# Kernel tuning notes

Measured on AMD Instinct MI355X. Metric: run time of the kernel, lower is better.

Reference implementation:

```python
import jax, jax.numpy as jnp
import numpy as np

# dims (match init_kwargs)
L, D, H, K = 8, 384, 6, 64            # layers, hidden, rwkv heads, rwkv head dim
DI, MH, HD, DS, CK = 768, 12, 64, 64, 4  # mamba: d_inner, heads, head_dim, d_state, conv kernel
V, B, T = 32000, 1, 1024


def _rms(x, w, eps=1e-6):
    return w * x * jax.lax.rsqrt(jnp.mean(x * x, axis=-1, keepdims=True) + eps)


def _rwkv6(xn, Wr, Wk, Wv, Wg, Ww, w_bias, u, gn_w, gn_b, Wo):
    # RWKV6: data-dependent diagonal-decay linear attention
    Bb, Tt, Dd = xn.shape
    proj = lambda W: (xn @ W).reshape(Bb, Tt, H, K)
    r, k, v = proj(Wr), proj(Wk), proj(Wv)
    g = xn @ Wg                                        # [B,T,D]
    w = (xn @ Ww + w_bias).reshape(Bb, Tt, H, K)
    decay = jnp.exp(-jnp.exp(w))                       # in (0,1)

    def step(S, inp):                                  # S: [B,H,K,K] (key x value)
        r_t, k_t, v_t, d_t = inp                       # each [B,H,K]
        kv = k_t[..., :, None] * v_t[..., None, :]     # [B,H,K,K]
        o = jnp.einsum('bhk,bhkv->bhv', r_t, S + u[None, :, :, None] * kv)
        S = d_t[..., None] * S + kv
        return S, o

    tm = lambda a: jnp.moveaxis(a, 1, 0)               # time-major
    S0 = jnp.zeros((Bb, H, K, K), xn.dtype)
    _, o = jax.lax.scan(step, S0, (tm(r), tm(k), tm(v), tm(decay)))
    o = jnp.moveaxis(o, 0, 1)                          # [B,T,H,K]
    # per-head GroupNorm
    mu = jnp.mean(o, -1, keepdims=True)
    var = jnp.var(o, -1, keepdims=True)
    o = (o - mu) * jax.lax.rsqrt(var + 1e-5) * gn_w.reshape(H, K) + gn_b.reshape(H, K)
    o = o.reshape(Bb, Tt, Dd) * jax.nn.silu(g)
    return o @ Wo


def _mamba2(xn, W_in, conv_w, conv_b, dt_bias, A_log, Dp, mn_w, W_out):
    # Mamba2: selective scan with scalar A per head
    Bb, Tt, Dd = xn.shape
    zxbcdt = xn @ W_in                                 # [B,T, 2*DI + 2*DS + MH]
    z = zxbcdt[..., :DI]
    xBC = zxbcdt[..., DI:DI + DI + 2 * DS]
    dt = jax.nn.softplus(zxbcdt[..., -MH:] + dt_bias)  # [B,T,MH]
    # causal depthwise conv1d, kernel CK
    xp = jnp.pad(xBC, ((0, 0), (CK - 1, 0), (0, 0)))
    xBC = sum(xp[:, j:j + Tt, :] * conv_w[:, j] for j in range(CK)) + conv_b
    xBC = jax.nn.silu(xBC)
    xs = xBC[..., :DI].reshape(Bb, Tt, MH, HD)
    Bm = xBC[..., DI:DI + DS]                          # [B,T,DS]
    Cm = xBC[..., DI + DS:]                            # [B,T,DS]
    A = -jnp.exp(A_log)                                # [MH]

    def step(S, inp):                                  # S: [B,MH,HD,DS]
        x_t, B_t, C_t, dt_t = inp                      # [B,MH,HD],[B,DS],[B,DS],[B,MH]
        dA = jnp.exp(dt_t * A)                         # [B,MH]
        S = dA[..., None, None] * S + (dt_t[..., None] * x_t)[..., None] * B_t[:, None, None, :]
        y = jnp.einsum('bhps,bs->bhp', S, C_t) + Dp[None, :, None] * x_t
        return S, y

    tm = lambda a: jnp.moveaxis(a, 1, 0)
    S0 = jnp.zeros((Bb, MH, HD, DS), xn.dtype)
    _, y = jax.lax.scan(step, S0, (tm(xs), tm(Bm), tm(Cm), tm(dt)))
    y = jnp.moveaxis(y, 0, 1).reshape(Bb, Tt, DI)
    y = _rms(y * jax.nn.silu(z), mn_w)                 # gated RMSNorm
    return y @ W_out


def _forward(x, embed, ln_w, Wr, Wk, Wv, Wg, Ww, w_bias, u, gn_w, gn_b, Wo,
             W_in, conv_w, conv_b, dt_bias, A_log, Dp, mn_w, W_out,
             gw, gb, ffn_ln_w, ffn_w1, ffn_w2, ln_out_w):
    h = jnp.take(embed, x, axis=0)                     # [B,T,D]
    for i in range(L):
        xn = _rms(h, ln_w[i])
        o_r = _rwkv6(xn, Wr[i], Wk[i], Wv[i], Wg[i], Ww[i], w_bias[i], u[i], gn_w[i], gn_b[i], Wo[i])
        o_m = _mamba2(xn, W_in[i], conv_w[i], conv_b[i], dt_bias[i], A_log[i], Dp[i], mn_w[i], W_out[i])
        gate = jax.nn.sigmoid(jnp.concatenate([o_r, o_m], -1) @ gw[i] + gb[i])  # [B,T,1]
        h = h + gate * o_r + (1.0 - gate) * o_m
        hn = _rms(h, ffn_ln_w[i])
        h = h + jax.nn.gelu(hn @ ffn_w1[i], approximate=False) @ ffn_w2[i]
    h = _rms(h, ln_out_w)
    return h @ embed.T                                 # tied head -> [B,T,V]


def setup_inputs() -> dict:
    key = jax.random.key(0)
    ks = iter(jax.random.split(key, 32))
    n = lambda shape, s=0.02: jax.random.normal(next(ks), shape, jnp.float32) * s
    d = {}
    d['x'] = jax.random.randint(next(ks), (B, T), 0, V)
    d['embed'] = n((V, D))
    d['ln_w'] = jnp.ones((L, D), jnp.float32)
    d['Wr'] = n((L, D, D)); d['Wk'] = n((L, D, D)); d['Wv'] = n((L, D, D))
    d['Wg'] = n((L, D, D)); d['Ww'] = n((L, D, D))
    d['w_bias'] = n((L, D), 0.5)
    d['u'] = n((L, H, K), 0.5)
    d['gn_w'] = jnp.ones((L, D), jnp.float32)
    d['gn_b'] = jnp.zeros((L, D), jnp.float32)
    d['Wo'] = n((L, D, D))
    d['W_in'] = n((L, D, 2 * DI + 2 * DS + MH))
    d['conv_w'] = n((L, DI + 2 * DS, CK), 0.2)
    d['conv_b'] = jnp.zeros((L, DI + 2 * DS), jnp.float32)
    d['dt_bias'] = jax.random.uniform(next(ks), (L, MH), jnp.float32, -4.0, -1.0)
    d['A_log'] = jnp.log(jax.random.uniform(next(ks), (L, MH), jnp.float32, 1.0, 16.0))
    d['Dp'] = jnp.ones((L, MH), jnp.float32)
    d['mn_w'] = jnp.ones((L, DI), jnp.float32)
    d['W_out'] = n((L, DI, D))
    d['gw'] = n((L, 2 * D, 1), 0.01)
    d['gb'] = jnp.full((L, 1), float(np.log(0.3 / 0.7)), jnp.float32)
    d['ffn_ln_w'] = jnp.ones((L, D), jnp.float32)
    d['ffn_w1'] = n((L, D, 4 * D))
    d['ffn_w2'] = n((L, 4 * D, D))
    d['ln_out_w'] = jnp.ones((D,), jnp.float32)
    return d


def reference(x, embed, ln_w, Wr, Wk, Wv, Wg, Ww, w_bias, u, gn_w, gn_b, Wo,
              W_in, conv_w, conv_b, dt_bias, A_log, Dp, mn_w, W_out,
              gw, gb, ffn_ln_w, ffn_w1, ffn_w2, ln_out_w):
    return _forward(x, embed, ln_w, Wr, Wk, Wv, Wg, Ww, w_bias, u, gn_w, gn_b, Wo,
                    W_in, conv_w, conv_b, dt_bias, A_log, Dp, mn_w, W_out,
                    gw, gb, ffn_ln_w, ffn_w1, ffn_w2, ln_out_w)
```

## Files before the change

### kernel.cpp

```cpp
#include <hip/hip_runtime.h>
#include <math.h>

#define TT 1024
#define DD 384
#define NH 6
#define DI 768
#define MH 12
#define DS 64
#define NL 8
#define XDIM 1676
#define CONVC 896
#define NV 32000
#define PZS 3712
#define G_OFF 1152
#define W_OFF 1536
#define Z_OFF 1920
#define XBC_OFF 2688
#define DT_OFF 3584
#define CHK 32
#define NCH 32

typedef __attribute__((ext_vector_type(8))) short short8;
typedef __attribute__((ext_vector_type(4))) float f32x4;

__device__ __forceinline__ float siluf(float x) { return x / (1.f + expf(-x)); }
__device__ __forceinline__ float sigmoidf_(float x) { return 1.f / (1.f + expf(-x)); }
__device__ __forceinline__ float geluf(float x) {
  return 0.5f * x * (1.f + erff(x * 0.70710678118654752440f));
}
__device__ __forceinline__ unsigned short f2b(float x) {
  union { float f; unsigned int u; } v; v.f = x;
  unsigned int r = v.u + 0x7fffu + ((v.u >> 16) & 1u);
  return (unsigned short)(r >> 16);
}

#define GLDS(gp, lp) __builtin_amdgcn_global_load_lds( \
    (const __attribute__((address_space(1))) void*)(gp), \
    (__attribute__((address_space(3))) void*)(lp), 16, 0, 0)

template<int EPI>
__global__ __launch_bounds__(256) void gemm_bf16(
    const unsigned short* __restrict__ A, const unsigned short* __restrict__ Bt,
    float* __restrict__ C, unsigned short* __restrict__ Cb, int N, int K, int ldC)
{
  __shared__ unsigned short As[2048];
  __shared__ unsigned short Bs[2048];
  int tid = threadIdx.x;
  int wid = tid >> 6, lane = tid & 63;
  int m0 = blockIdx.y * 64, n0 = blockIdx.x * 64;
  int wr = wid >> 1, wc = wid & 1;
  int sr = tid >> 2;
  int scs = ((tid & 3) ^ ((sr >> 1) & 3)) * 8;
  const unsigned short* ga = A  + (size_t)(m0 + sr) * K + scs;
  const unsigned short* gb = Bt + (size_t)(n0 + sr) * K + scs;
  unsigned short* la = As + wid * 512;
  unsigned short* lb = Bs + wid * 512;
  int fr = lane & 15, fc = lane >> 4;
  f32x4 zz = {0.f, 0.f, 0.f, 0.f};
  f32x4 acc[2][2];
  acc[0][0] = zz; acc[0][1] = zz; acc[1][0] = zz; acc[1][1] = zz;

  for (int k0 = 0; k0 < K; k0 += 32) {
    GLDS(ga + k0, la);
    GLDS(gb + k0, lb);
    __syncthreads();
    short8 af[2], bf[2];
#pragma unroll
    for (int mg = 0; mg < 2; ++mg) {
      int ar = wr * 32 + mg * 16 + fr;
      af[mg] = *reinterpret_cast<const short8*>(&As[ar * 32 + ((fc ^ ((ar >> 1) & 3)) * 8)]);
    }
#pragma unroll
    for (int ng = 0; ng < 2; ++ng) {
      int br = wc * 32 + ng * 16 + fr;
      bf[ng] = *reinterpret_cast<const short8*>(&Bs[br * 32 + ((fc ^ ((br >> 1) & 3)) * 8)]);
    }
#pragma unroll
    for (int mg = 0; mg < 2; ++mg)
#pragma unroll
      for (int ng = 0; ng < 2; ++ng)
        acc[mg][ng] = __builtin_amdgcn_mfma_f32_16x16x32_bf16(af[mg], bf[ng], acc[mg][ng], 0, 0, 0);
    __syncthreads();
  }
#pragma unroll
  for (int mg = 0; mg < 2; ++mg)
#pragma unroll
    for (int ng = 0; ng < 2; ++ng) {
      int col = n0 + wc * 32 + ng * 16 + fr;
      if (col < N) {
#pragma unroll
        for (int j = 0; j < 4; ++j) {
          int row = m0 + wr * 32 + mg * 16 + fc * 4 + j;
          if (EPI == 1)      Cb[(size_t)row * ldC + col] = f2b(geluf(acc[mg][ng][j]));
          else if (EPI == 2) C[(size_t)row * ldC + col] += acc[mg][ng][j];
          else               C[(size_t)row * ldC + col]  = acc[mg][ng][j];
        }
      }
    }
}

__global__ __launch_bounds__(256) void gemm128(
    const unsigned short* __restrict__ A, const unsigned short* __restrict__ Bt,
    float* __restrict__ C, int N, int K, int ldC)
{
  __shared__ unsigned short As[4096];
  __shared__ unsigned short Bs[4096];
  int tid = threadIdx.x;
  int wid = tid >> 6, lane = tid & 63;
  int m0 = blockIdx.y * 128, n0 = blockIdx.x * 128;
  int wr = wid >> 1, wc = wid & 1;
  int r0 = tid >> 2;
  int scs = ((tid & 3) ^ ((r0 >> 1) & 3)) * 8;
  const unsigned short* ga0 = A  + (size_t)(m0 + r0) * K + scs;
  const unsigned short* gb0 = Bt + (size_t)(n0 + r0) * K + scs;
  const unsigned short* ga1 = ga0 + (size_t)64 * K;
  const unsigned short* gb1 = gb0 + (size_t)64 * K;
  unsigned short* la0 = As + wid * 512;
  unsigned short* lb0 = Bs + wid * 512;
  unsigned short* la1 = As + 2048 + wid * 512;
  unsigned short* lb1 = Bs + 2048 + wid * 512;
  int fr = lane & 15, fc = lane >> 4;
  f32x4 zz = {0.f, 0.f, 0.f, 0.f};
  f32x4 acc[4][4];
#pragma unroll
  for (int i = 0; i < 4; i++)
#pragma unroll
    for (int j = 0; j < 4; j++) acc[i][j] = zz;

  for (int k0 = 0; k0 < K; k0 += 32) {
    GLDS(ga0 + k0, la0);
    GLDS(gb0 + k0, lb0);
    GLDS(ga1 + k0, la1);
    GLDS(gb1 + k0, lb1);
    __syncthreads();
    short8 af[4], bf[4];
#pragma unroll
    for (int mg = 0; mg < 4; ++mg) {
      int ar = wr * 64 + mg * 16 + fr;
      af[mg] = *reinterpret_cast<const short8*>(&As[ar * 32 + ((fc ^ ((ar >> 1) & 3)) * 8)]);
    }
#pragma unroll
    for (int ng = 0; ng < 4; ++ng) {
      int br = wc * 64 + ng * 16 + fr;
      bf[ng] = *reinterpret_cast<const short8*>(&Bs[br * 32 + ((fc ^ ((br >> 1) & 3)) * 8)]);
    }
#pragma unroll
    for (int mg = 0; mg < 4; ++mg)
#pragma unroll
      for (int ng = 0; ng < 4; ++ng)
        acc[mg][ng] = __builtin_amdgcn_mfma_f32_16x16x32_bf16(af[mg], bf[ng], acc[mg][ng], 0, 0, 0);
    __syncthreads();
  }
#pragma unroll
  for (int mg = 0; mg < 4; ++mg)
#pragma unroll
    for (int ng = 0; ng < 4; ++ng) {
      int col = n0 + wc * 64 + ng * 16 + fr;
      if (col < N) {
#pragma unroll
        for (int j = 0; j < 4; ++j) {
          int row = m0 + wr * 64 + mg * 16 + fc * 4 + j;
          C[(size_t)row * ldC + col] = acc[mg][ng][j];
        }
      }
    }
}

__global__ __launch_bounds__(256) void transconv_kernel(
    const float* __restrict__ src, unsigned short* __restrict__ dst,
    int K, int N, int Npad, size_t srcStride, size_t dstStride)
{
  __shared__ float tile[32][33];
  src += (size_t)blockIdx.z * srcStride;
  dst += (size_t)blockIdx.z * dstStride;
  int k0 = blockIdx.y * 32, n0 = blockIdx.x * 32;
  int tx = threadIdx.x & 31, ty = threadIdx.x >> 5;
  for (int i = ty; i < 32; i += 8) {
    int k = k0 + i, n = n0 + tx;
    tile[i][tx] = (k < K && n < N) ? src[(size_t)k * N + n] : 0.f;
  }
  __syncthreads();
  for (int i = ty; i < 32; i += 8) {
    int n = n0 + i, k = k0 + tx;
    if (n < Npad && k < K) dst[(size_t)n * K + k] = f2b(tile[tx][i]);
  }
}

__global__ void conv_b16_kernel(const float* __restrict__ src, unsigned short* __restrict__ dst, int n)
{
  int idx = blockIdx.x * 256 + threadIdx.x;
  if (idx < n) dst[idx] = f2b(src[idx]);
}

__global__ void embed_kernel(const int* __restrict__ x, const float* __restrict__ embed,
                             float* __restrict__ h)
{
  int idx = blockIdx.x * 256 + threadIdx.x;
  if (idx < TT * DD) {
    int t = idx / DD, d = idx % DD;
    h[idx] = embed[(size_t)x[t] * DD + d];
  }
}

__global__ __launch_bounds__(256) void rms_kernel(const float* __restrict__ in,
                                                  const float* __restrict__ w,
                                                  unsigned short* __restrict__ out,
                                                  int ncol, float eps)
{
  int t = blockIdx.x;
  const float* row = in + (size_t)t * ncol;
  float ss = 0.f;
  for (int c = threadIdx.x; c < ncol; c += 256) { float v = row[c]; ss = fmaf(v, v, ss); }
  __shared__ float red[256];
  red[threadIdx.x] = ss; __syncthreads();
  for (int s = 128; s > 0; s >>= 1) {
    if (threadIdx.x < s) red[threadIdx.x] += red[threadIdx.x + s];
    __syncthreads();
  }
  float scale = rsqrtf(red[0] / ncol + eps);
  for (int c = threadIdx.x; c < ncol; c += 256) out[(size_t)t * ncol + c] = f2b(w[c] * row[c] * scale);
}

__global__ __launch_bounds__(256) void scanA_kernel(
    const float* __restrict__ PZ, const float* __restrict__ u, const float* __restrict__ wbias,
    float* __restrict__ so, float* __restrict__ rPb,
    float* __restrict__ MstR, float* __restrict__ DcR,
    const float* __restrict__ xbc, const float* __restrict__ dtbias,
    const float* __restrict__ Alog, const float* __restrict__ Dpw,
    float* __restrict__ yb, float* __restrict__ Ccb,
    float* __restrict__ MstM, float* __restrict__ DcM)
{
  __shared__ float smem[2 * 256 + 64];
  int b = blockIdx.x, tid = threadIdx.x;
  if (b < 192) {
    int h = b >> 5, c = b & 31;
    float* sbuf = smem; float* us = smem + 512;
    if (tid < 64) us[tid] = u[h * 64 + tid];
    int wv = tid >> 6, l = tid & 63;
    int vv = wv * 16 + (l & 15);
    int kc = l >> 4;
    int arr = tid >> 6, idx = tid & 63;
    int off = (arr == 0) ? 0 : (arr == 1) ? 384 : (arr == 2) ? W_OFF : 768;
    float wb = (arr == 2) ? wbias[h * 64 + idx] : 0.f;
    size_t base = (size_t)h * 64 + idx + off;
    int t0 = c * CHK;
    float S[16], Pc[16];
#pragma unroll
    for (int i = 0; i < 16; i++) { S[i] = 0.f; Pc[i] = 1.f; }
    float reg = PZ[(size_t)t0 * PZS + base];
    bool st = (wv == 0) && ((l & 15) == 0);
    for (int t = 0; t < CHK; ++t) {
      int tt = t0 + t;
      float* cb = sbuf + (t & 1) * 256;
      cb[arr * 64 + idx] = (arr == 2) ? expf(-expf(reg + wb)) : reg;
      if (t + 1 < CHK) reg = PZ[(size_t)(tt + 1) * PZS + base];
      __syncthreads();
      float vt = cb[192 + vv];
      float acc = 0.f;
      float rp[16];
#pragma unroll
      for (int i = 0; i < 16; ++i) {
        int kk = kc * 16 + i;
        float rv = cb[kk], kv = cb[64 + kk], dv = cb[128 + kk];
        rp[i] = rv * Pc[i];
        float kvv = kv * vt;
        acc = fmaf(rv, fmaf(us[kk], kvv, S[i]), acc);
        S[i] = fmaf(dv, S[i], kvv);
        Pc[i] *= dv;
      }
      acc += __shfl_xor(acc, 16);
      acc += __shfl_xor(acc, 32);
      if (l < 16) so[(size_t)tt * DD + h * 64 + vv] = acc;
      if (st) {
        float4* dst = (float4*)&rPb[(size_t)tt * DD + h * 64 + kc * 16];
        dst[0] = make_float4(rp[0], rp[1], rp[2], rp[3]);
        dst[1] = make_float4(rp[4], rp[5], rp[6], rp[7]);
        dst[2] = make_float4(rp[8], rp[9], rp[10], rp[11]);
        dst[3] = make_float4(rp[12], rp[13], rp[14], rp[15]);
      }
    }
    float* ms = MstR + (size_t)(h * NCH + c) * 4096;
    float4* msv = (float4*)&ms[vv * 64 + kc * 16];
    msv[0] = make_float4(S[0], S[1], S[2], S[3]);
    msv[1] = make_float4(S[4], S[5], S[6], S[7]);
    msv[2] = make_float4(S[8], S[9], S[10], S[11]);
    msv[3] = make_float4(S[12], S[13], S[14], S[15]);
    if (st) {
      float4* dd_ = (float4*)&DcR[(h * NCH + c) * 64 + kc * 16];
      dd_[0] = make_float4(Pc[0], Pc[1], Pc[2], Pc[3]);
      dd_[1] = make_float4(Pc[4], Pc[5], Pc[6], Pc[7]);
      dd_[2] = make_float4(Pc[8], Pc[9], Pc[10], Pc[11]);
      dd_[3] = make_float4(Pc[12], Pc[13], Pc[14], Pc[15]);
    }
  } else {
    int bb = b - 192;
    int hh = bb >> 5, c = bb & 31;
    float* sbuf = smem;
    int wv = tid >> 6, l = tid & 63;
    int p = wv * 16 + (l & 15);
    int sc = l >> 4;
    int arr = tid >> 6, idx = tid & 63;
    float A = -expf(Alog[hh]);
    float Dph = Dpw[hh];
    float dtbh = dtbias[hh];
    int off = (arr == 0) ? (hh * 64 + idx) : (arr == 1) ? (DI + idx) : (DI + DS + idx);
    int t0 = c * CHK;
    float S[16]; float cdA = 1.f;
#pragma unroll
    for (int i = 0; i < 16; i++) S[i] = 0.f;
    float reg = (arr < 3) ? xbc[(size_t)t0 * CONVC + off]
                          : PZ[(size_t)t0 * PZS + DT_OFF + hh];
    bool st = (wv == 0) && ((l & 15) == 0);
    for (int t = 0; t < CHK; ++t) {
      int tt = t0 + t;
      float* cb = sbuf + (t & 1) * 256;
      if (arr < 3) cb[arr * 64 + idx] = reg;
      else if (idx == 0) {
        float v = reg + dtbh;
        cb[192] = (v > 20.f) ? v : log1pf(expf(v));
      }
      if (t + 1 < CHK) reg = (arr < 3) ? xbc[(size_t)(tt + 1) * CONVC + off]
                                       : PZ[(size_t)(tt + 1) * PZS + DT_OFF + hh];
      __syncthreads();
      float dt_ = cb[192];
      float dA = expf(dt_ * A);
      cdA *= dA;
      float xp = cb[p];
      float dtx = dt_ * xp;
      float acc = 0.f;
#pragma unroll
      for (int i = 0; i < 16; ++i) {
        int s = sc * 16 + i;
        S[i] = fmaf(dA, S[i], dtx * cb[64 + s]);
        acc = fmaf(S[i], cb[128 + s], acc);
      }
      acc += __shfl_xor(acc, 16);
      acc += __shfl_xor(acc, 32);
      if (l < 16) yb[(size_t)tt * DI + hh * 64 + p] = fmaf(Dph, xp, acc);
      if (st) {
        float4* dst = (float4*)&Ccb[(size_t)tt * DI + hh * 64 + sc * 16];
#pragma unroll
        for (int j4 = 0; j4 < 4; ++j4)
          dst[j4] = make_float4(cdA * cb[128 + sc * 16 + j4 * 4 + 0],
                                cdA * cb[128 + sc * 16 + j4 * 4 + 1],
                                cdA * cb[128 + sc * 16 + j4 * 4 + 2],
                                cdA * cb[128 + sc * 16 + j4 * 4 + 3]);
      }
    }
    float* ms = MstM + (size_t)(hh * NCH + c) * 4096;
    float4* msv = (float4*)&ms[p * 64 + sc * 16];
    msv[0] = make_float4(S[0], S[1], S[2], S[3]);
    msv[1] = make_float4(S[4], S[5], S[6], S[7]);
    msv[2] = make_float4(S[8], S[9], S[10], S[11]);
    msv[3] = make_float4(S[12], S[13], S[14], S[15]);
    if (tid == 0) DcM[hh * NCH + c] = cdA;
  }
}

__global__ __launch_bounds__(256) void combine_kernel(
    const float* __restrict__ MstR, const float* __restrict__ DcR, float* __restrict__ S0R,
    const float* __restrict__ MstM, const float* __restrict__ DcM, float* __restrict__ S0M)
{
  int b = blockIdx.x, tid = threadIdx.x;
  if (b < 96) {
    int h = b >> 4, sub = b & 15;
    int ei = sub * 256 + tid;
    int k = ei & 63;
    float S = 0.f;
#pragma unroll
    for (int c = 0; c < NCH; ++c) {
      size_t base = (size_t)(h * NCH + c) * 4096;
      float m = MstR[base + ei];
      float dD = DcR[(h * NCH + c) * 64 + k];
      S0R[base + ei] = S;
      S = fmaf(dD, S, m);
    }
  } else {
    int bb = b - 96;
    int hh = bb >> 4, sub = bb & 15;
    int ei = sub * 256 + tid;
    float S = 0.f;
#pragma unroll
    for (int c = 0; c < NCH; ++c) {
      size_t base = (size_t)(hh * NCH + c) * 4096;
      float m = MstM[base + ei];
      float dD = DcM[hh * NCH + c];
      S0M[base + ei] = S;
      S = fmaf(dD, S, m);
    }
  }
}

__global__ __launch_bounds__(256) void corr_kernel(
    const float* __restrict__ S0R, const float* __restrict__ rPb, const float* __restrict__ so,
    const float* __restrict__ S0M, const float* __restrict__ Ccb, float* __restrict__ yb,
    const float* __restrict__ PZ, const float* __restrict__ gnw, const float* __restrict__ gnb,
    unsigned short* __restrict__ gob)
{
  __shared__ float S0l[64 * 68];
  __shared__ float Rl[CHK * 68];
  int b = blockIdx.x, tid = threadIdx.x;
  const float* s0g; const float* rg; int ostride, obase, t0;
  bool rwkv = (b < 192);
  int h;
  if (rwkv) {
    h = b >> 5; int c = b & 31; t0 = c * CHK;
    s0g = S0R + (size_t)(h * NCH + c) * 4096;
    rg = rPb; obase = h * 64; ostride = DD;
  } else {
    int bb = b - 192; h = bb >> 5; int c = bb & 31; t0 = c * CHK;
    s0g = S0M + (size_t)(h * NCH + c) * 4096;
    rg = Ccb; obase = h * 64; ostride = DI;
  }
  for (int gi = tid; gi < 4096; gi += 256)
    S0l[(gi & 63) * 68 + (gi >> 6)] = s0g[gi];
  {
    int t = tid >> 3, q = (tid & 7) * 8;
    const float4* src = (const float4*)&rg[(size_t)(t0 + t) * ostride + obase + q];
    float4* dst = (float4*)&Rl[t * 68 + q];
    dst[0] = src[0]; dst[1] = src[1];
  }
  __syncthreads();
  int t = tid >> 3, q = (tid & 7) * 8;
  float acc[8];
#pragma unroll
  for (int j = 0; j < 8; j++) acc[j] = 0.f;
  for (int k = 0; k < 64; ++k) {
    float rv = Rl[t * 68 + k];
    const float4* sp = (const float4*)&S0l[k * 68 + q];
    float4 s0 = sp[0], s1 = sp[1];
    acc[0] = fmaf(rv, s0.x, acc[0]);
    acc[1] = fmaf(rv, s0.y, acc[1]);
    acc[2] = fmaf(rv, s0.z, acc[2]);
    acc[3] = fmaf(rv, s0.w, acc[3]);
    acc[4] = fmaf(rv, s1.x, acc[4]);
    acc[5] = fmaf(rv, s1.y, acc[5]);
    acc[6] = fmaf(rv, s1.z, acc[6]);
    acc[7] = fmaf(rv, s1.w, acc[7]);
  }
  if (!rwkv) {
    float4* op = (float4*)&yb[(size_t)(t0 + t) * DI + obase + q];
    float4 c0 = op[0], c1 = op[1];
    c0.x += acc[0]; c0.y += acc[1]; c0.z += acc[2]; c0.w += acc[3];
    c1.x += acc[4]; c1.y += acc[5]; c1.z += acc[6]; c1.w += acc[7];
    op[0] = c0; op[1] = c1;
  } else {
    float ov[8];
    const float4* sp = (const float4*)&so[(size_t)(t0 + t) * DD + obase + q];
    float4 s0 = sp[0], s1 = sp[1];
    ov[0] = s0.x + acc[0]; ov[1] = s0.y + acc[1]; ov[2] = s0.z + acc[2]; ov[3] = s0.w + acc[3];
    ov[4] = s1.x + acc[4]; ov[5] = s1.y + acc[5]; ov[6] = s1.z + acc[6]; ov[7] = s1.w + acc[7];
    float m_ = 0.f;
#pragma unroll
    for (int j = 0; j < 8; j++) m_ += ov[j];
    m_ += __shfl_xor(m_, 1); m_ += __shfl_xor(m_, 2); m_ += __shfl_xor(m_, 4);
    float mu = m_ * (1.f / 64.f);
    float vv = 0.f;
#pragma unroll
    for (int j = 0; j < 8; j++) { float d = ov[j] - mu; vv = fmaf(d, d, vv); }
    vv += __shfl_xor(vv, 1); vv += __shfl_xor(vv, 2); vv += __shfl_xor(vv, 4);
    float rstd = rsqrtf(vv * (1.f / 64.f) + 1e-5f);
#pragma unroll
    for (int j = 0; j < 8; j++) {
      int d = obase + q + j;
      float gv = PZ[(size_t)(t0 + t) * PZS + G_OFF + d];
      float o = fmaf((ov[j] - mu) * rstd, gnw[d], gnb[d]) * siluf(gv);
      gob[(size_t)(t0 + t) * DD + d] = f2b(o);
    }
  }
}

__global__ void conv_kernel(const float* __restrict__ PZ, const float* __restrict__ cw,
                            const float* __restrict__ cb, float* __restrict__ out)
{
  int idx = blockIdx.x * 256 + threadIdx.x;
  if (idx >= TT * CONVC) return;
  int t = idx / CONVC, c = idx % CONVC;
  float acc = cb[c];
#pragma unroll
  for (int j = 0; j < 4; ++j) {
    int tt = t + j - 3;
    if (tt >= 0) acc = fmaf(PZ[(size_t)tt * PZS + XBC_OFF + c], cw[c * 4 + j], acc);
  }
  out[idx] = siluf(acc);
}

__global__ __launch_bounds__(256) void mamba_norm_kernel(const float* __restrict__ yb,
    const float* __restrict__ PZ, const float* __restrict__ mnw, unsigned short* __restrict__ out)
{
  int t = blockIdx.x;
  __shared__ float vbuf[DI];
  __shared__ float red[256];
  float ss = 0.f;
  for (int c = threadIdx.x; c < DI; c += 256) {
    float z = PZ[(size_t)t * PZS + Z_OFF + c];
    float v = yb[(size_t)t * DI + c] * siluf(z);
    vbuf[c] = v;
    ss = fmaf(v, v, ss);
  }
  red[threadIdx.x] = ss; __syncthreads();
  for (int s = 128; s > 0; s >>= 1) {
    if (threadIdx.x < s) red[threadIdx.x] += red[threadIdx.x + s];
    __syncthreads();
  }
  float scale = rsqrtf(red[0] / DI + 1e-6f);
  for (int c = threadIdx.x; c < DI; c += 256)
    out[(size_t)t * DI + c] = f2b(vbuf[c] * scale * mnw[c]);
}

__global__ __launch_bounds__(256) void gate_rms_kernel(const float* __restrict__ orb,
    const float* __restrict__ omb, const float* __restrict__ gw,
    const float* __restrict__ gb, const float* __restrict__ flnw,
    float* __restrict__ h, unsigned short* __restrict__ xnb)
{
  int t = blockIdx.x;
  __shared__ float red[256];
  __shared__ float vbuf[DD];
  float ss = 0.f;
  for (int c = threadIdx.x; c < DD; c += 256)
    ss += orb[(size_t)t * DD + c] * gw[c] + omb[(size_t)t * DD + c] * gw[DD + c];
  red[threadIdx.x] = ss; __syncthreads();
  for (int s = 128; s > 0; s >>= 1) {
    if (threadIdx.x < s) red[threadIdx.x] += red[threadIdx.x + s];
    __syncthreads();
  }
  float gate = sigmoidf_(red[0] + gb[0]);
  __syncthreads();
  float ss2 = 0.f;
  for (int c = threadIdx.x; c < DD; c += 256) {
    size_t ix = (size_t)t * DD + c;
    float hn = h[ix] + gate * orb[ix] + (1.f - gate) * omb[ix];
    h[ix] = hn; vbuf[c] = hn;
    ss2 = fmaf(hn, hn, ss2);
  }
  red[threadIdx.x] = ss2; __syncthreads();
  for (int s = 128; s > 0; s >>= 1) {
    if (threadIdx.x < s) red[threadIdx.x] += red[threadIdx.x + s];
    __syncthreads();
  }
  float scale = rsqrtf(red[0] / DD + 1e-6f);
  for (int c = threadIdx.x; c < DD; c += 256)
    xnb[(size_t)t * DD + c] = f2b(flnw[c] * vbuf[c] * scale);
}

extern "C" void kernel_launch(void* const* d_in, const int* in_sizes, int n_in,
                              void* d_out, int out_size, void* d_ws, size_t ws_size,
                              hipStream_t stream)
{
  const int*   x        = (const int*)  d_in[0];
  const float* embed    = (const float*)d_in[1];
  const float* ln_w     = (const float*)d_in[2];
  const float* Wr       = (const float*)d_in[3];
  const float* Wk       = (const float*)d_in[4];
  const float* Wv       = (const float*)d_in[5];
  const float* Wg       = (const float*)d_in[6];
  const float* Ww       = (const float*)d_in[7];
  const float* w_bias   = (const float*)d_in[8];
  const float* u        = (const float*)d_in[9];
  const float* gn_w     = (const float*)d_in[10];
  const float* gn_b     = (const float*)d_in[11];
  const float* Wo       = (const float*)d_in[12];
  const float* W_in     = (const float*)d_in[13];
  const float* conv_w   = (const float*)d_in[14];
  const float* conv_b   = (const float*)d_in[15];
  const float* dt_bias  = (const float*)d_in[16];
  const float* A_log    = (const float*)d_in[17];
  const float* Dp       = (const float*)d_in[18];
  const float* mn_w     = (const float*)d_in[19];
  const float* W_out    = (const float*)d_in[20];
  const float* gw       = (const float*)d_in[21];
  const float* gb       = (const float*)d_in[22];
  const float* ffn_ln_w = (const float*)d_in[23];
  const float* ffn_w1   = (const float*)d_in[24];
  const float* ffn_w2   = (const float*)d_in[25];
  const float* ln_out_w = (const float*)d_in[26];

  char* base = (char*)d_ws;
  size_t off = 0;
  auto alloc = [&](size_t bytes) { off = (off + 255) & ~(size_t)255; void* p = base + off; off += bytes; return p; };

  float* h    = (float*)alloc((size_t)TT * DD * 4);
  float* PZ   = (float*)alloc((size_t)TT * PZS * 4);
  float* xb   = (float*)alloc((size_t)TT * CONVC * 4);
  float* yb   = (float*)alloc((size_t)TT * DI * 4);
  float* so   = (float*)alloc((size_t)TT * DD * 4);
  float* orb  = (float*)alloc((size_t)TT * DD * 4);
  float* omb  = (float*)alloc((size_t)TT * DD * 4);
  float* rPb  = (float*)alloc((size_t)TT * DD * 4);
  float* Ccb  = (float*)alloc((size_t)TT * DI * 4);
  float* MstR = (float*)alloc((size_t)NH * NCH * 4096 * 4);
  float* DcR  = (float*)alloc((size_t)NH * NCH * 64 * 4);
  float* S0R  = (float*)alloc((size_t)NH * NCH * 4096 * 4);
  float* MstM = (float*)alloc((size_t)MH * NCH * 4096 * 4);
  float* DcM  = (float*)alloc((size_t)MH * NCH * 4);
  float* S0M  = (float*)alloc((size_t)MH * NCH * 4096 * 4);
  unsigned short* xnb = (unsigned short*)alloc((size_t)TT * DD * 2);
  unsigned short* gob = (unsigned short*)alloc((size_t)TT * DD * 2);
  unsigned short* ynb = (unsigned short*)alloc((size_t)TT * DI * 2);
  unsigned short* fhb = (unsigned short*)alloc((size_t)TT * 1536 * 2);
  unsigned short* WallT = (unsigned short*)alloc((size_t)NL * PZS * 384 * 2);
  unsigned short* WoT   = (unsigned short*)alloc((size_t)NL * 384 * 384 * 2);
  unsigned short* WoutT = (unsigned short*)alloc((size_t)NL * 384 * 768 * 2);
  unsigned short* F1T   = (unsigned short*)alloc((size_t)NL * 1536 * 384 * 2);
  unsigned short* F2T   = (unsigned short*)alloc((size_t)NL * 384 * 1536 * 2);
  unsigned short* embB  = (unsigned short*)alloc((size_t)NV * DD * 2);
  (void)ws_size; (void)in_sizes; (void)n_in; (void)out_size;

  dim3 blk(256);
  int gTD = (TT * DD + 255) / 256;

  const float* Wrkvgw[5] = {Wr, Wk, Wv, Wg, Ww};
  for (int j = 0; j < 5; ++j)
    transconv_kernel<<<dim3(12, 12, 8), blk, 0, stream>>>(
        Wrkvgw[j], WallT + (size_t)j * 384 * 384, 384, 384, 384,
        (size_t)384 * 384, (size_t)PZS * 384);
  transconv_kernel<<<dim3(56, 12, 8), blk, 0, stream>>>(
      W_in, WallT + (size_t)1920 * 384, 384, XDIM, 1792,
      (size_t)384 * XDIM, (size_t)PZS * 384);
  transconv_kernel<<<dim3(12, 12, 8), blk, 0, stream>>>(
      Wo, WoT, 384, 384, 384, (size_t)384 * 384, (size_t)384 * 384);
  transconv_kernel<<<dim3(12, 24, 8), blk, 0, stream>>>(
      W_out, WoutT, 768, 384, 384, (size_t)768 * 384, (size_t)384 * 768);
  transconv_kernel<<<dim3(48, 12, 8), blk, 0, stream>>>(
      ffn_w1, F1T, 384, 1536, 1536, (size_t)384 * 1536, (size_t)1536 * 384);
  transconv_kernel<<<dim3(12, 48, 8), blk, 0, stream>>>(
      ffn_w2, F2T, 1536, 384, 384, (size_t)1536 * 384, (size_t)384 * 1536);
  conv_b16_kernel<<<(NV * DD + 255) / 256, blk, 0, stream>>>(embed, embB, NV * DD);

  embed_kernel<<<gTD, blk, 0, stream>>>(x, embed, h);

  for (int i = 0; i < NL; ++i) {
    rms_kernel<<<TT, blk, 0, stream>>>(h, ln_w + (size_t)i * DD, xnb, DD, 1e-6f);

    gemm_bf16<0><<<dim3(58, 16), blk, 0, stream>>>(
        xnb, WallT + (size_t)i * PZS * 384, PZ, nullptr, PZS, 384, PZS);
    conv_kernel<<<(TT * CONVC + 255) / 256, blk, 0, stream>>>(
        PZ, conv_w + (size_t)i * CONVC * 4, conv_b + (size_t)i * CONVC, xb);

    scanA_kernel<<<576, blk, 0, stream>>>(PZ, u + (size_t)i * NH * 64, w_bias + (size_t)i * DD,
                                          so, rPb, MstR, DcR,
                                          xb, dt_bias + (size_t)i * MH,
                                          A_log + (size_t)i * MH, Dp + (size_t)i * MH,
                                          yb, Ccb, MstM, DcM);
    combine_kernel<<<288, blk, 0, stream>>>(MstR, DcR, S0R, MstM, DcM, S0M);
    corr_kernel<<<576, blk, 0, stream>>>(S0R, rPb, so, S0M, Ccb, yb,
                                         PZ, gn_w + (size_t)i * DD, gn_b + (size_t)i * DD, gob);

    gemm_bf16<0><<<dim3(6, 16), blk, 0, stream>>>(
        gob, WoT + (size_t)i * 384 * 384, orb, nullptr, DD, 384, DD);

    mamba_norm_kernel<<<TT, blk, 0, stream>>>(yb, PZ, mn_w + (size_t)i * DI, ynb);
    gemm_bf16<0><<<dim3(6, 16), blk, 0, stream>>>(
        ynb, WoutT + (size_t)i * 384 * 768, omb, nullptr, DD, 768, DD);

    gate_rms_kernel<<<TT, blk, 0, stream>>>(orb, omb, gw + (size_t)i * 2 * DD, gb + i,
                                            ffn_ln_w + (size_t)i * DD, h, xnb);

    gemm_bf16<1><<<dim3(24, 16), blk, 0, stream>>>(
        xnb, F1T + (size_t)i * 1536 * 384, nullptr, fhb, 1536, 384, 1536);
    gemm_bf16<2><<<dim3(6, 16), blk, 0, stream>>>(
        fhb, F2T + (size_t)i * 384 * 1536, h, nullptr, DD, 1536, DD);
  }

  rms_kernel<<<TT, blk, 0, stream>>>(h, ln_out_w, xnb, DD, 1e-6f);
  gemm128<<<dim3(250, 8), blk, 0, stream>>>(
      xnb, embB, (float*)d_out, NV, 384, NV);
}
```

Measured before the change: 1.184 ms.

## Fuse conv into scan, merge output GEMMs, split-K FFN2, warp-per-row norms

Several independent changes land together. The causal depthwise conv plus SiLU moves into the Mamba scan kernel as a per-thread sliding window, which removes the separate conv kernel and the xb buffer. The two small output projections (RWKV Wo and Mamba W_out) now run in one dual-GEMM launch. The FFN down-projection uses a 4-way split-K with atomicAdd into h to fill more CUs. The RMS, mamba-norm and gate-RMS kernels switch to one wavefront per row with shuffle reductions instead of shared-memory tree reductions. The atomic accumulation makes summation order nondeterministic.

```diff
diff --git a/kernel.cpp b/kernel.cpp
--- a/kernel.cpp
+++ b/kernel.cpp
@@ -60,6 +60,73 @@
   f32x4 acc[2][2];
   acc[0][0] = zz; acc[0][1] = zz; acc[1][0] = zz; acc[1][1] = zz;
 
+  int kper = K / (int)gridDim.z;
+  int ks = blockIdx.z * kper, ke = ks + kper;
+  for (int k0 = ks; k0 < ke; k0 += 32) {
+    GLDS(ga + k0, la);
+    GLDS(gb + k0, lb);
+    __syncthreads();
+    short8 af[2], bf[2];
+#pragma unroll
+    for (int mg = 0; mg < 2; ++mg) {
+      int ar = wr * 32 + mg * 16 + fr;
+      af[mg] = *reinterpret_cast<const short8*>(&As[ar * 32 + ((fc ^ ((ar >> 1) & 3)) * 8)]);
+    }
+#pragma unroll
+    for (int ng = 0; ng < 2; ++ng) {
+      int br = wc * 32 + ng * 16 + fr;
+      bf[ng] = *reinterpret_cast<const short8*>(&Bs[br * 32 + ((fc ^ ((br >> 1) & 3)) * 8)]);
+    }
+#pragma unroll
+    for (int mg = 0; mg < 2; ++mg)
+#pragma unroll
+      for (int ng = 0; ng < 2; ++ng)
+        acc[mg][ng] = __builtin_amdgcn_mfma_f32_16x16x32_bf16(af[mg], bf[ng], acc[mg][ng], 0, 0, 0);
+    __syncthreads();
+  }
+#pragma unroll
+  for (int mg = 0; mg < 2; ++mg)
+#pragma unroll
+    for (int ng = 0; ng < 2; ++ng) {
+      int col = n0 + wc * 32 + ng * 16 + fr;
+      if (col < N) {
+#pragma unroll
+        for (int j = 0; j < 4; ++j) {
+          int row = m0 + wr * 32 + mg * 16 + fc * 4 + j;
+          if (EPI == 1)      Cb[(size_t)row * ldC + col] = f2b(geluf(acc[mg][ng][j]));
+          else if (EPI == 3) atomicAdd(&C[(size_t)row * ldC + col], acc[mg][ng][j]);
+          else               C[(size_t)row * ldC + col]  = acc[mg][ng][j];
+        }
+      }
+    }
+}
+
+__global__ __launch_bounds__(256) void gemm_dual(
+    const unsigned short* __restrict__ A0, const unsigned short* __restrict__ B0t,
+    float* __restrict__ C0, int K0, int ld0, int nx0, int nb0,
+    const unsigned short* __restrict__ A1, const unsigned short* __restrict__ B1t,
+    float* __restrict__ C1, int K1, int ld1, int nx1)
+{
+  __shared__ unsigned short As[2048];
+  __shared__ unsigned short Bs[2048];
+  int b = blockIdx.x;
+  const unsigned short *A, *Bt; float* C; int K, ldC, bx, by;
+  if (b < nb0) { A = A0; Bt = B0t; C = C0; K = K0; ldC = ld0; bx = b % nx0; by = b / nx0; }
+  else { b -= nb0; A = A1; Bt = B1t; C = C1; K = K1; ldC = ld1; bx = b % nx1; by = b / nx1; }
+  int tid = threadIdx.x;
+  int wid = tid >> 6, lane = tid & 63;
+  int m0 = by * 64, n0 = bx * 64;
+  int wr = wid >> 1, wc = wid & 1;
+  int sr = tid >> 2;
+  int scs = ((tid & 3) ^ ((sr >> 1) & 3)) * 8;
+  const unsigned short* ga = A  + (size_t)(m0 + sr) * K + scs;
+  const unsigned short* gb = Bt + (size_t)(n0 + sr) * K + scs;
+  unsigned short* la = As + wid * 512;
+  unsigned short* lb = Bs + wid * 512;
+  int fr = lane & 15, fc = lane >> 4;
+  f32x4 zz = {0.f, 0.f, 0.f, 0.f};
+  f32x4 acc[2][2];
+  acc[0][0] = zz; acc[0][1] = zz; acc[1][0] = zz; acc[1][1] = zz;
   for (int k0 = 0; k0 < K; k0 += 32) {
     GLDS(ga + k0, la);
     GLDS(gb + k0, lb);
@@ -87,14 +154,10 @@
 #pragma unroll
     for (int ng = 0; ng < 2; ++ng) {
       int col = n0 + wc * 32 + ng * 16 + fr;
-      if (col < N) {
-#pragma unroll
-        for (int j = 0; j < 4; ++j) {
-          int row = m0 + wr * 32 + mg * 16 + fc * 4 + j;
-          if (EPI == 1)      Cb[(size_t)row * ldC + col] = f2b(geluf(acc[mg][ng][j]));
-          else if (EPI == 2) C[(size_t)row * ldC + col] += acc[mg][ng][j];
-          else               C[(size_t)row * ldC + col]  = acc[mg][ng][j];
-        }
+#pragma unroll
+      for (int j = 0; j < 4; ++j) {
+        int row = m0 + wr * 32 + mg * 16 + fc * 4 + j;
+        C[(size_t)row * ldC + col] = acc[mg][ng][j];
       }
     }
 }
@@ -204,28 +267,28 @@
 
 __global__ __launch_bounds__(256) void rms_kernel(const float* __restrict__ in,
                                                   const float* __restrict__ w,
-                                                  unsigned short* __restrict__ out,
-                                                  int ncol, float eps)
-{
-  int t = blockIdx.x;
-  const float* row = in + (size_t)t * ncol;
-  float ss = 0.f;
-  for (int c = threadIdx.x; c < ncol; c += 256) { float v = row[c]; ss = fmaf(v, v, ss); }
-  __shared__ float red[256];
-  red[threadIdx.x] = ss; __syncthreads();
-  for (int s = 128; s > 0; s >>= 1) {
-    if (threadIdx.x < s) red[threadIdx.x] += red[threadIdx.x + s];
-    __syncthreads();
-  }
-  float scale = rsqrtf(red[0] / ncol + eps);
-  for (int c = threadIdx.x; c < ncol; c += 256) out[(size_t)t * ncol + c] = f2b(w[c] * row[c] * scale);
+                                                  unsigned short* __restrict__ out)
+{
+  int row = blockIdx.x * 4 + (threadIdx.x >> 6);
+  int lane = threadIdx.x & 63;
+  const float* r = in + (size_t)row * DD;
+  float v[6]; float ss = 0.f;
+#pragma unroll
+  for (int j = 0; j < 6; ++j) { v[j] = r[lane + j * 64]; ss = fmaf(v[j], v[j], ss); }
+#pragma unroll
+  for (int s = 1; s < 64; s <<= 1) ss += __shfl_xor(ss, s);
+  float scale = rsqrtf(ss * (1.f / DD) + 1e-6f);
+#pragma unroll
+  for (int j = 0; j < 6; ++j)
+    out[(size_t)row * DD + lane + j * 64] = f2b(w[lane + j * 64] * v[j] * scale);
 }
 
 __global__ __launch_bounds__(256) void scanA_kernel(
     const float* __restrict__ PZ, const float* __restrict__ u, const float* __restrict__ wbias,
     float* __restrict__ so, float* __restrict__ rPb,
     float* __restrict__ MstR, float* __restrict__ DcR,
-    const float* __restrict__ xbc, const float* __restrict__ dtbias,
+    const float* __restrict__ cw, const float* __restrict__ cbia,
+    const float* __restrict__ dtbias,
     const float* __restrict__ Alog, const float* __restrict__ Dpw,
     float* __restrict__ yb, float* __restrict__ Ccb,
     float* __restrict__ MstM, float* __restrict__ DcM)
@@ -303,24 +366,42 @@
     float A = -expf(Alog[hh]);
     float Dph = Dpw[hh];
     float dtbh = dtbias[hh];
-    int off = (arr == 0) ? (hh * 64 + idx) : (arr == 1) ? (DI + idx) : (DI + DS + idx);
     int t0 = c * CHK;
+    float cw0 = 0.f, cw1 = 0.f, cw2 = 0.f, cw3 = 0.f, cbv = 0.f;
+    float xw0 = 0.f, xw1 = 0.f, xw2 = 0.f, cur = 0.f;
+    const float* xcol = nullptr;
+    float reg = 0.f;
+    if (arr < 3) {
+      int ch = (arr == 0) ? (hh * 64 + idx) : (arr == 1) ? (DI + idx) : (DI + DS + idx);
+      cw0 = cw[ch * 4 + 0]; cw1 = cw[ch * 4 + 1]; cw2 = cw[ch * 4 + 2]; cw3 = cw[ch * 4 + 3];
+      cbv = cbia[ch];
+      xcol = PZ + XBC_OFF + ch;
+      xw0 = (t0 >= 3) ? xcol[(size_t)(t0 - 3) * PZS] : 0.f;
+      xw1 = (t0 >= 2) ? xcol[(size_t)(t0 - 2) * PZS] : 0.f;
+      xw2 = (t0 >= 1) ? xcol[(size_t)(t0 - 1) * PZS] : 0.f;
+      cur = xcol[(size_t)t0 * PZS];
+    } else {
+      reg = PZ[(size_t)t0 * PZS + DT_OFF + hh];
+    }
     float S[16]; float cdA = 1.f;
 #pragma unroll
     for (int i = 0; i < 16; i++) S[i] = 0.f;
-    float reg = (arr < 3) ? xbc[(size_t)t0 * CONVC + off]
-                          : PZ[(size_t)t0 * PZS + DT_OFF + hh];
     bool st = (wv == 0) && ((l & 15) == 0);
     for (int t = 0; t < CHK; ++t) {
       int tt = t0 + t;
       float* cb = sbuf + (t & 1) * 256;
-      if (arr < 3) cb[arr * 64 + idx] = reg;
-      else if (idx == 0) {
-        float v = reg + dtbh;
-        cb[192] = (v > 20.f) ? v : log1pf(expf(v));
+      if (arr < 3) {
+        float cvv = fmaf(cw3, cur, fmaf(cw2, xw2, fmaf(cw1, xw1, fmaf(cw0, xw0, cbv))));
+        cb[arr * 64 + idx] = siluf(cvv);
+        float nx = (t + 1 < CHK) ? xcol[(size_t)(tt + 1) * PZS] : 0.f;
+        xw0 = xw1; xw1 = xw2; xw2 = cur; cur = nx;
+      } else {
+        if (idx == 0) {
+          float v = reg + dtbh;
+          cb[192] = (v > 20.f) ? v : log1pf(expf(v));
+        }
+        if (t + 1 < CHK) reg = PZ[(size_t)(tt + 1) * PZS + DT_OFF + hh];
       }
-      if (t + 1 < CHK) reg = (arr < 3) ? xbc[(size_t)(tt + 1) * CONVC + off]
-                                       : PZ[(size_t)(tt + 1) * PZS + DT_OFF + hh];
       __syncthreads();
       float dt_ = cb[192];
       float dA = expf(dt_ * A);
@@ -470,42 +551,27 @@
   }
 }
 
-__global__ void conv_kernel(const float* __restrict__ PZ, const float* __restrict__ cw,
-                            const float* __restrict__ cb, float* __restrict__ out)
-{
-  int idx = blockIdx.x * 256 + threadIdx.x;
-  if (idx >= TT * CONVC) return;
-  int t = idx / CONVC, c = idx % CONVC;
-  float acc = cb[c];
-#pragma unroll
-  for (int j = 0; j < 4; ++j) {
-    int tt = t + j - 3;
-    if (tt >= 0) acc = fmaf(PZ[(size_t)tt * PZS + XBC_OFF + c], cw[c * 4 + j], acc);
-  }
-  out[idx] = siluf(acc);
-}
-
 __global__ __launch_bounds__(256) void mamba_norm_kernel(const float* __restrict__ yb,
     const float* __restrict__ PZ, const float* __restrict__ mnw, unsigned short* __restrict__ out)
 {
-  int t = blockIdx.x;
-  __shared__ float vbuf[DI];
-  __shared__ float red[256];
-  float ss = 0.f;
-  for (int c = threadIdx.x; c < DI; c += 256) {
-    float z = PZ[(size_t)t * PZS + Z_OFF + c];
-    float v = yb[(size_t)t * DI + c] * siluf(z);
-    vbuf[c] = v;
-    ss = fmaf(v, v, ss);
-  }
-  red[threadIdx.x] = ss; __syncthreads();
-  for (int s = 128; s > 0; s >>= 1) {
-    if (threadIdx.x < s) red[threadIdx.x] += red[threadIdx.x + s];
-    __syncthreads();
-  }
-  float scale = rsqrtf(red[0] / DI + 1e-6f);
-  for (int c = threadIdx.x; c < DI; c += 256)
-    out[(size_t)t * DI + c] = f2b(vbuf[c] * scale * mnw[c]);
+  int row = blockIdx.x * 4 + (threadIdx.x >> 6);
+  int lane = threadIdx.x & 63;
+  float v[12]; float ss = 0.f;
+#pragma unroll
+  for (int j = 0; j < 12; ++j) {
+    int c = lane + j * 64;
+    float z = PZ[(size_t)row * PZS + Z_OFF + c];
+    float t = yb[(size_t)row * DI + c] * siluf(z);
+    v[j] = t; ss = fmaf(t, t, ss);
+  }
+#pragma unroll
+  for (int s = 1; s < 64; s <<= 1) ss += __shfl_xor(ss, s);
+  float scale = rsqrtf(ss * (1.f / DI) + 1e-6f);
+#pragma unroll
+  for (int j = 0; j < 12; ++j) {
+    int c = lane + j * 64;
+    out[(size_t)row * DI + c] = f2b(v[j] * scale * mnw[c]);
+  }
 }
 
 __global__ __launch_bounds__(256) void gate_rms_kernel(const float* __restrict__ orb,
@@ -513,34 +579,35 @@
     const float* __restrict__ gb, const float* __restrict__ flnw,
     float* __restrict__ h, unsigned short* __restrict__ xnb)
 {
-  int t = blockIdx.x;
-  __shared__ float red[256];
-  __shared__ float vbuf[DD];
-  float ss = 0.f;
-  for (int c = threadIdx.x; c < DD; c += 256)
-    ss += orb[(size_t)t * DD + c] * gw[c] + omb[(size_t)t * DD + c] * gw[DD + c];
-  red[threadIdx.x] = ss; __syncthreads();
-  for (int s = 128; s > 0; s >>= 1) {
-    if (threadIdx.x < s) red[threadIdx.x] += red[threadIdx.x + s];
-    __syncthreads();
-  }
-  float gate = sigmoidf_(red[0] + gb[0]);
-  __syncthreads();
-  float ss2 = 0.f;
-  for (int c = threadIdx.x; c < DD; c += 256) {
-    size_t ix = (size_t)t * DD + c;
-    float hn = h[ix] + gate * orb[ix] + (1.f - gate) * omb[ix];
-    h[ix] = hn; vbuf[c] = hn;
-    ss2 = fmaf(hn, hn, ss2);
-  }
-  red[threadIdx.x] = ss2; __syncthreads();
-  for (int s = 128; s > 0; s >>= 1) {
-    if (threadIdx.x < s) red[threadIdx.x] += red[threadIdx.x + s];
-    __syncthreads();
-  }
-  float scale = rsqrtf(red[0] / DD + 1e-6f);
-  for (int c = threadIdx.x; c < DD; c += 256)
-    xnb[(size_t)t * DD + c] = f2b(flnw[c] * vbuf[c] * scale);
+  int row = blockIdx.x * 4 + (threadIdx.x >> 6);
+  int lane = threadIdx.x & 63;
+  float a[6], bq[6]; float ss = 0.f;
+#pragma unroll
+  for (int j = 0; j < 6; ++j) {
+    int c = lane + j * 64;
+    a[j] = orb[(size_t)row * DD + c]; bq[j] = omb[(size_t)row * DD + c];
+    ss += a[j] * gw[c] + bq[j] * gw[DD + c];
+  }
+#pragma unroll
+  for (int s = 1; s < 64; s <<= 1) ss += __shfl_xor(ss, s);
+  float gate = sigmoidf_(ss + gb[0]);
+  float hn[6]; float ss2 = 0.f;
+#pragma unroll
+  for (int j = 0; j < 6; ++j) {
+    int c = lane + j * 64;
+    size_t ix = (size_t)row * DD + c;
+    hn[j] = h[ix] + gate * a[j] + (1.f - gate) * bq[j];
+    h[ix] = hn[j];
+    ss2 = fmaf(hn[j], hn[j], ss2);
+  }
+#pragma unroll
+  for (int s = 1; s < 64; s <<= 1) ss2 += __shfl_xor(ss2, s);
+  float scale = rsqrtf(ss2 * (1.f / DD) + 1e-6f);
+#pragma unroll
+  for (int j = 0; j < 6; ++j) {
+    int c = lane + j * 64;
+    xnb[(size_t)row * DD + c] = f2b(flnw[c] * hn[j] * scale);
+  }
 }
 
 extern "C" void kernel_launch(void* const* d_in, const int* in_sizes, int n_in,
@@ -581,7 +648,6 @@
 
   float* h    = (float*)alloc((size_t)TT * DD * 4);
   float* PZ   = (float*)alloc((size_t)TT * PZS * 4);
-  float* xb   = (float*)alloc((size_t)TT * CONVC * 4);
   float* yb   = (float*)alloc((size_t)TT * DI * 4);
   float* so   = (float*)alloc((size_t)TT * DD * 4);
   float* orb  = (float*)alloc((size_t)TT * DD * 4);
@@ -630,39 +696,37 @@
   embed_kernel<<<gTD, blk, 0, stream>>>(x, embed, h);
 
   for (int i = 0; i < NL; ++i) {
-    rms_kernel<<<TT, blk, 0, stream>>>(h, ln_w + (size_t)i * DD, xnb, DD, 1e-6f);
+    rms_kernel<<<256, blk, 0, stream>>>(h, ln_w + (size_t)i * DD, xnb);
 
     gemm_bf16<0><<<dim3(58, 16), blk, 0, stream>>>(
         xnb, WallT + (size_t)i * PZS * 384, PZ, nullptr, PZS, 384, PZS);
-    conv_kernel<<<(TT * CONVC + 255) / 256, blk, 0, stream>>>(
-        PZ, conv_w + (size_t)i * CONVC * 4, conv_b + (size_t)i * CONVC, xb);
 
     scanA_kernel<<<576, blk, 0, stream>>>(PZ, u + (size_t)i * NH * 64, w_bias + (size_t)i * DD,
                                           so, rPb, MstR, DcR,
-                                          xb, dt_bias + (size_t)i * MH,
+                                          conv_w + (size_t)i * CONVC * 4, conv_b + (size_t)i * CONVC,
+                                          dt_bias + (size_t)i * MH,
                                           A_log + (size_t)i * MH, Dp + (size_t)i * MH,
                                           yb, Ccb, MstM, DcM);
     combine_kernel<<<288, blk, 0, stream>>>(MstR, DcR, S0R, MstM, DcM, S0M);
     corr_kernel<<<576, blk, 0, stream>>>(S0R, rPb, so, S0M, Ccb, yb,
                                          PZ, gn_w + (size_t)i * DD, gn_b + (size_t)i * DD, gob);
 
-    gemm_bf16<0><<<dim3(6, 16), blk, 0, stream>>>(
-        gob, WoT + (size_t)i * 384 * 384, orb, nullptr, DD, 384, DD);
-
-    mamba_norm_kernel<<<TT, blk, 0, stream>>>(yb, PZ, mn_w + (size_t)i * DI, ynb);
-    gemm_bf16<0><<<dim3(6, 16), blk, 0, stream>>>(
-        ynb, WoutT + (size_t)i * 384 * 768, omb, nullptr, DD, 768, DD);
-
-    gate_rms_kernel<<<TT, blk, 0, stream>>>(orb, omb, gw + (size_t)i * 2 * DD, gb + i,
-                                            ffn_ln_w + (size_t)i * DD, h, xnb);
+    mamba_norm_kernel<<<256, blk, 0, stream>>>(yb, PZ, mn_w + (size_t)i * DI, ynb);
+
+    gemm_dual<<<192, blk, 0, stream>>>(
+        gob, WoT + (size_t)i * 384 * 384, orb, 384, DD, 6, 96,
+        ynb, WoutT + (size_t)i * 384 * 768, omb, 768, DD, 6);
+
+    gate_rms_kernel<<<256, blk, 0, stream>>>(orb, omb, gw + (size_t)i * 2 * DD, gb + i,
+                                             ffn_ln_w + (size_t)i * DD, h, xnb);
 
     gemm_bf16<1><<<dim3(24, 16), blk, 0, stream>>>(
         xnb, F1T + (size_t)i * 1536 * 384, nullptr, fhb, 1536, 384, 1536);
-    gemm_bf16<2><<<dim3(6, 16), blk, 0, stream>>>(
+    gemm_bf16<3><<<dim3(6, 16, 4), blk, 0, stream>>>(
         fhb, F2T + (size_t)i * 384 * 1536, h, nullptr, DD, 1536, DD);
   }
 
-  rms_kernel<<<TT, blk, 0, stream>>>(h, ln_out_w, xnb, DD, 1e-6f);
+  rms_kernel<<<256, blk, 0, stream>>>(h, ln_out_w, xnb);
   gemm128<<<dim3(250, 8), blk, 0, stream>>>(
       xnb, embB, (float*)d_out, NV, 384, NV);
 }
```

Result: faster. 980.6 us (-17.2%).
